# Kernel optimization log

Measured on AMD Instinct MI355X. Metric: run time of the kernel, lower is better.

Reference implementation:

```python
import jax, jax.numpy as jnp
import numpy as np

DEPTH, DIM, M_DIM, K = 3, 16, 16, 8  # depth, emb_dim, EGNN m_dim default, num_nearest_neighbors
LN_EPS = 1e-5


def _gather(x, idx):
    # x: [B,L,...], idx: [B,L,K] -> [B,L,K,...] (per-batch neighbor gather)
    return jax.vmap(lambda xb, ib: xb[ib])(x, idx)


def _lin(k, fi, fo):
    k1, k2 = jax.random.split(k)
    lim = 1.0 / np.sqrt(fi)
    w = jax.random.uniform(k1, (fi, fo), minval=-lim, maxval=lim, dtype=jnp.float32)
    b = jax.random.uniform(k2, (fo,), minval=-lim, maxval=lim, dtype=jnp.float32)
    return w, b


def _stacked(k, fi, fo):
    ws, bs = zip(*[_lin(kk, fi, fo) for kk in jax.random.split(k, DEPTH)])
    return jnp.stack(ws), jnp.stack(bs)


def setup_inputs() -> dict:
    key = jax.random.key(0)
    ks = jax.random.split(key, 16)
    B, L, num_tokens = 16, 1024, 2
    edge_in = 2 * DIM + 1  # feats_i, feats_j, rel_dist
    inp = {}
    inp['coords'] = jax.random.normal(ks[0], (B, L, 3), dtype=jnp.float32) * 3.0
    inp['residues'] = jax.random.randint(ks[1], (B, L), 0, num_tokens)
    inp['lengths'] = jax.random.randint(ks[2], (B,), L // 2, L + 1)
    inp['token_emb'] = jax.random.normal(ks[3], (num_tokens, DIM), dtype=jnp.float32)
    inp['pos_emb'] = jax.random.normal(ks[4], (L, DIM), dtype=jnp.float32)
    inp['edge_w1'], inp['edge_b1'] = _stacked(ks[5], edge_in, edge_in * 2)
    inp['edge_w2'], inp['edge_b2'] = _stacked(ks[6], edge_in * 2, M_DIM)
    inp['coors_w1'], inp['coors_b1'] = _stacked(ks[7], M_DIM, M_DIM * 4)
    inp['coors_w2'], inp['coors_b2'] = _stacked(ks[8], M_DIM * 4, 1)
    inp['ln_g'] = jnp.ones((DEPTH, DIM), jnp.float32)
    inp['ln_b'] = jnp.zeros((DEPTH, DIM), jnp.float32)
    inp['node_w1'], inp['node_b1'] = _stacked(ks[9], DIM + M_DIM, DIM * 2)
    inp['node_w2'], inp['node_b2'] = _stacked(ks[10], DIM * 2, DIM)
    inp['final_w'], inp['final_b'] = _lin(ks[11], DIM, 3)
    return inp


def reference(coords, residues, lengths, token_emb, pos_emb,
              edge_w1, edge_b1, edge_w2, edge_b2,
              coors_w1, coors_b1, coors_w2, coors_b2,
              ln_g, ln_b, node_w1, node_b1, node_w2, node_b2,
              final_w, final_b):
    B, L, _ = coords.shape
    silu = jax.nn.silu
    mask = jnp.arange(L)[None, :] < lengths[:, None]                 # [B,L]
    pair_mask = mask[:, :, None] & mask[:, None, :]                  # [B,L,L]
    eye = jnp.eye(L, dtype=bool)
    # chain adjacency: i <-> i+1 where both endpoints are within length
    r = jnp.arange(L - 1)
    chain = jnp.zeros((L, L), bool).at[r, r + 1].set(True)
    chain = chain | chain.T
    adj = (chain[None] & pair_mask) & ~eye                           # [B,L,L]

    feats = token_emb[residues] + pos_emb[None, :L]                  # [B,L,D]
    coors = coords
    for d in range(DEPTH):
        # pairwise squared distances for kNN ranking (memory-bound)
        rel_dist_full = jnp.sum((coors[:, :, None] - coors[:, None, :]) ** 2, -1)  # [B,L,L]
        ranking = jnp.where(pair_mask, rel_dist_full, 1e5)
        ranking = jnp.where(eye, -1.0, ranking)   # self always selected first
        ranking = jnp.where(adj, 0.0, ranking)    # adjacency edges forced in
        _, idx = jax.lax.top_k(-ranking, K)                           # [B,L,K] smallest
        mask_j = _gather(mask, idx)
        emask = mask[:, :, None] & mask_j                             # [B,L,K] (valid_radius=inf)
        coors_j = _gather(coors, idx)                                 # [B,L,K,3]
        rel_coors = coors[:, :, None] - coors_j                       # [B,L,K,3]
        rel_dist = jnp.sum(rel_coors ** 2, -1, keepdims=True)         # [B,L,K,1]
        feats_j = _gather(feats, idx)                                 # [B,L,K,D]
        feats_i = jnp.broadcast_to(feats[:, :, None], feats_j.shape)
        edge_in = jnp.concatenate([feats_i, feats_j, rel_dist], -1)   # [B,L,K,2D+1]
        h = silu(edge_in @ edge_w1[d] + edge_b1[d])
        m_ij = silu(h @ edge_w2[d] + edge_b2[d])                      # [B,L,K,M]
        # equivariant coordinate update
        w = silu(m_ij @ coors_w1[d] + coors_b1[d]) @ coors_w2[d] + coors_b2[d]
        w = jnp.where(emask[..., None], w, 0.0)[..., 0]               # [B,L,K]
        coors = coors + jnp.einsum('blk,blkc->blc', w, rel_coors)
        # node update (norm_feats=True in EGNN_Network -> LayerNorm)
        m_i = jnp.sum(jnp.where(emask[..., None], m_ij, 0.0), 2)      # [B,L,M]
        mu = feats.mean(-1, keepdims=True)
        var = jnp.mean((feats - mu) ** 2, -1, keepdims=True)
        normed = (feats - mu) / jnp.sqrt(var + LN_EPS) * ln_g[d] + ln_b[d]
        nin = jnp.concatenate([normed, m_i], -1)                      # [B,L,D+M]
        feats = feats + (silu(nin @ node_w1[d] + node_b1[d]) @ node_w2[d] + node_b2[d])
    delta = feats @ final_w + final_b                                 # [B,L,3]
    return delta
```

## Files before the change

### kernel.cpp

```cpp
#include <hip/hip_runtime.h>
#include <math.h>

typedef unsigned long long u64;
typedef unsigned int u32;

#define NB 16
#define SL 1024
#define DIM 16
#define MDIM 16
#define KNN 8
#define EH 66
#define CH 64
#define NHID 32
#define LN_EPS 1e-5f
#define W1T_STRIDE 36

__device__ __forceinline__ float silu_f(float x) {
    return x / (1.0f + __expf(-x));
}

__global__ __launch_bounds__(256) void init_kernel(
    const float* __restrict__ coords, const int* __restrict__ residues,
    const float* __restrict__ token_emb, const float* __restrict__ pos_emb,
    float* __restrict__ coordsA, float* __restrict__ featsA)
{
    const int nid = blockIdx.x * 256 + threadIdx.x;
    if (nid >= NB * SL) return;
    const int l = nid & (SL - 1);
    const int r = residues[nid];
#pragma unroll
    for (int c = 0; c < DIM; ++c)
        featsA[nid * DIM + c] = token_emb[r * DIM + c] + pos_emb[l * DIM + c];
#pragma unroll
    for (int c = 0; c < 3; ++c)
        coordsA[nid * 3 + c] = coords[nid * 3 + c];
}

__global__ __launch_bounds__(256) void pack_kernel(
    const float* __restrict__ ew1, const float* __restrict__ cw1,
    const float* __restrict__ nw1, const float* __restrict__ nw2,
    float* __restrict__ w1t, float* __restrict__ cw1t,
    float* __restrict__ nw1t, float* __restrict__ nw2t)
{
    const int stride = gridDim.x * 256;
    const int t0 = blockIdx.x * 256 + threadIdx.x;
    for (int idx = t0; idx < 3 * EH * 33; idx += stride) {
        int d = idx / (EH * 33); int r = idx - d * EH * 33; int u = r / 33; int c = r - u * 33;
        w1t[(d * EH + u) * W1T_STRIDE + c] = ew1[(d * 33 + c) * EH + u];
    }
    for (int idx = t0; idx < 3 * CH * 16; idx += stride) {
        int d = idx / (CH * 16); int r = idx - d * CH * 16; int t = r >> 4; int v = r & 15;
        cw1t[(d * CH + t) * 16 + v] = cw1[(d * 16 + v) * CH + t];
    }
    for (int idx = t0; idx < 3 * NHID * 32; idx += stride) {
        int d = idx / (NHID * 32); int r = idx - d * NHID * 32; int u = r >> 5; int c = r & 31;
        nw1t[(d * NHID + u) * 32 + c] = nw1[(d * 32 + c) * NHID + u];
    }
    for (int idx = t0; idx < 3 * 16 * 32; idx += stride) {
        int d = idx / (16 * 32); int r = idx - d * 16 * 32; int c = r >> 5; int u = r & 31;
        nw2t[(d * 16 + c) * 32 + u] = nw2[(d * 32 + u) * 16 + c];
    }
}

__device__ __forceinline__ void merge8(u32* a, const u32* bb) {
    u32 c[8];
#pragma unroll
    for (int t = 0; t < 8; ++t) c[t] = min(a[t], bb[7 - t]);
#define MCAS(x, y) { u32 mn = min(c[x], c[y]); u32 mx = max(c[x], c[y]); c[x] = mn; c[y] = mx; }
    MCAS(0, 4) MCAS(1, 5) MCAS(2, 6) MCAS(3, 7)
    MCAS(0, 2) MCAS(1, 3) MCAS(4, 6) MCAS(5, 7)
    MCAS(0, 1) MCAS(2, 3) MCAS(4, 5) MCAS(6, 7)
#undef MCAS
#pragma unroll
    for (int t = 0; t < 8; ++t) a[t] = c[t];
}

__global__ __launch_bounds__(1024) void knn_kernel(
    const float* __restrict__ coords, const int* __restrict__ lengths,
    int* __restrict__ idxbuf)
{
    __shared__ float s_cand[SL * 3];
    __shared__ u32 lists[16][64][9];
    const int tid = threadIdx.x;
    const int b = blockIdx.x >> 4;
    const int i0 = (blockIdx.x & 15) << 6;
    const int len = lengths[b];
    const float* cb = coords + (size_t)b * SL * 3;
    for (int idx = tid; idx < SL * 3; idx += 1024) s_cand[idx] = cb[idx];
    __syncthreads();

    const int wv = tid >> 6;
    const int lane = tid & 63;
    const int i = i0 + lane;
    const bool mi = i < len;
    const float xi = s_cand[i * 3 + 0], yi = s_cand[i * 3 + 1], zi = s_cand[i * 3 + 2];

    u32 lst[8];
#pragma unroll
    for (int t = 0; t < 8; ++t) lst[t] = 0xFFFFFFFFu;

    const int jbase = wv << 6;
#pragma unroll 4
    for (int jj = 0; jj < 64; ++jj) {
        const int j = jbase + jj;
        const float xj = s_cand[j * 3 + 0], yj = s_cand[j * 3 + 1], zj = s_cand[j * 3 + 2];
        const float dx = xi - xj, dy = yi - yj, dz = zi - zj;
        const float dist = dx * dx + dy * dy + dz * dz;
        const bool pm = mi && (j < len);
        float v = pm ? dist : 1e5f;
        v = (pm && (j - i == 1 || i - j == 1)) ? 0.0f : v;
        v = (j == i) ? -1.0f : v;
        u32 bits = __float_as_uint(v);
        bits ^= (u32)((int)bits >> 31) | 0x80000000u;
        const u32 key = (bits & 0xFFFFFC00u) | (u32)j;
#pragma unroll
        for (int p = 7; p >= 1; --p)
            lst[p] = (key < lst[p]) ? ((key < lst[p - 1]) ? lst[p - 1] : key) : lst[p];
        lst[0] = min(key, lst[0]);
    }

#pragma unroll
    for (int t = 0; t < 8; ++t) lists[wv][lane][t] = lst[t];
    __syncthreads();

    if (tid < 512) {
        const int p = tid >> 6, q = tid & 63;
        u32 a[8], bb[8];
#pragma unroll
        for (int t = 0; t < 8; ++t) { a[t] = lists[2 * p][q][t]; bb[t] = lists[2 * p + 1][q][t]; }
        merge8(a, bb);
#pragma unroll
        for (int t = 0; t < 8; ++t) lists[2 * p][q][t] = a[t];
    }
    __syncthreads();
    if (tid < 256) {
        const int p = tid >> 6, q = tid & 63;
        u32 a[8], bb[8];
#pragma unroll
        for (int t = 0; t < 8; ++t) { a[t] = lists[4 * p][q][t]; bb[t] = lists[4 * p + 2][q][t]; }
        merge8(a, bb);
#pragma unroll
        for (int t = 0; t < 8; ++t) lists[4 * p][q][t] = a[t];
    }
    __syncthreads();
    if (tid < 128) {
        const int p = tid >> 6, q = tid & 63;
        u32 a[8], bb[8];
#pragma unroll
        for (int t = 0; t < 8; ++t) { a[t] = lists[8 * p][q][t]; bb[t] = lists[8 * p + 4][q][t]; }
        merge8(a, bb);
#pragma unroll
        for (int t = 0; t < 8; ++t) lists[8 * p][q][t] = a[t];
    }
    __syncthreads();
    if (tid < 64) {
        const int q = tid;
        u32 a[8], bb[8];
#pragma unroll
        for (int t = 0; t < 8; ++t) { a[t] = lists[0][q][t]; bb[t] = lists[8][q][t]; }
        merge8(a, bb);
        const size_t node = (size_t)b * SL + i0 + q;
        int4 r0 = make_int4((int)(a[0] & 1023u), (int)(a[1] & 1023u), (int)(a[2] & 1023u), (int)(a[3] & 1023u));
        int4 r1 = make_int4((int)(a[4] & 1023u), (int)(a[5] & 1023u), (int)(a[6] & 1023u), (int)(a[7] & 1023u));
        ((int4*)idxbuf)[node * 2 + 0] = r0;
        ((int4*)idxbuf)[node * 2 + 1] = r1;
    }
}

__global__ __launch_bounds__(256, 4) void layer_kernel(
    const int d,
    const float* __restrict__ coordsIn, float* __restrict__ coordsOut,
    const float* __restrict__ featsIn, float* __restrict__ featsOut,
    const int* __restrict__ idxbuf, const int* __restrict__ lengths,
    const float* __restrict__ w1t, const float* __restrict__ g_eb1,
    const float* __restrict__ g_ew2, const float* __restrict__ g_eb2,
    const float* __restrict__ cw1t, const float* __restrict__ g_cb1,
    const float* __restrict__ g_cw2, const float* __restrict__ g_cb2,
    const float* __restrict__ g_lng, const float* __restrict__ g_lnb,
    const float* __restrict__ nw1t, const float* __restrict__ g_nb1,
    const float* __restrict__ nw2t, const float* __restrict__ g_nb2)
{
    __shared__ float s_w1[EH * 36];
    __shared__ float s_w2e[EH * 16];
    __shared__ float s_cw1[CH * 16];
    __shared__ float s_cw2v[CH];
    __shared__ float s_nw1[NHID * 36];
    __shared__ float s_nw2[16 * 36];
    __shared__ float s_eb1[EH], s_eb2[16], s_cb1[CH];
    __shared__ float s_lng[16], s_lnb[16], s_nb1[32], s_nb2[16];
    __shared__ float s_cb2v;
    __shared__ __align__(16) float s_ex[2 * 64 * 20];

    const int tid = threadIdx.x;
    for (int t = tid; t < EH * 36; t += 256) s_w1[t] = w1t[d * EH * 36 + t];
    for (int t = tid; t < EH * 16; t += 256) s_w2e[t] = g_ew2[d * EH * 16 + t];
    for (int t = tid; t < CH * 16; t += 256) s_cw1[t] = cw1t[d * CH * 16 + t];
    for (int t = tid; t < NHID * 32; t += 256) s_nw1[(t >> 5) * 36 + (t & 31)] = nw1t[d * NHID * 32 + t];
    for (int t = tid; t < 16 * 32; t += 256) s_nw2[(t >> 5) * 36 + (t & 31)] = nw2t[d * 16 * 32 + t];
    if (tid < CH) { s_cw2v[tid] = g_cw2[d * CH + tid]; s_cb1[tid] = g_cb1[d * CH + tid]; }
    if (tid < EH) s_eb1[tid] = g_eb1[d * EH + tid];
    if (tid < 16) {
        s_eb2[tid] = g_eb2[d * 16 + tid];
        s_lng[tid] = g_lng[d * 16 + tid];
        s_lnb[tid] = g_lnb[d * 16 + tid];
        s_nb2[tid] = g_nb2[d * 16 + tid];
    }
    if (tid < 32) s_nb1[tid] = g_nb1[d * 32 + tid];
    if (tid == 0) s_cb2v = g_cb2[d];

    const int wvid = tid >> 6;
    const int h = wvid & 1;
    const int p = wvid >> 1;
    const int lane = tid & 63;
    const int e = blockIdx.x * 128 + p * 64 + lane;
    const int n = e >> 3;
    const int b = n >> 10;
    const int i = n & (SL - 1);
    const int k = lane & 7;
    const int len = lengths[b];
    const int j = idxbuf[e];
    const bool em = (i < len) && (j < len);

    float fi[16], fj[16];
    {
        const float4* pp = (const float4*)(featsIn + (size_t)n * DIM);
        float4 a = pp[0], c2 = pp[1], c3 = pp[2], c4 = pp[3];
        fi[0]=a.x; fi[1]=a.y; fi[2]=a.z; fi[3]=a.w;
        fi[4]=c2.x; fi[5]=c2.y; fi[6]=c2.z; fi[7]=c2.w;
        fi[8]=c3.x; fi[9]=c3.y; fi[10]=c3.z; fi[11]=c3.w;
        fi[12]=c4.x; fi[13]=c4.y; fi[14]=c4.z; fi[15]=c4.w;
    }
    {
        const float4* pp = (const float4*)(featsIn + ((size_t)b * SL + j) * DIM);
        float4 a = pp[0], c2 = pp[1], c3 = pp[2], c4 = pp[3];
        fj[0]=a.x; fj[1]=a.y; fj[2]=a.z; fj[3]=a.w;
        fj[4]=c2.x; fj[5]=c2.y; fj[6]=c2.z; fj[7]=c2.w;
        fj[8]=c3.x; fj[9]=c3.y; fj[10]=c3.z; fj[11]=c3.w;
        fj[12]=c4.x; fj[13]=c4.y; fj[14]=c4.z; fj[15]=c4.w;
    }
    float ci[3], rel[3];
    {
        const float* cp = coordsIn + (size_t)n * 3;
        const float* cq = coordsIn + ((size_t)b * SL + j) * 3;
        ci[0] = cp[0]; ci[1] = cp[1]; ci[2] = cp[2];
        rel[0] = ci[0] - cq[0]; rel[1] = ci[1] - cq[1]; rel[2] = ci[2] - cq[2];
    }
    const float rd = fmaf(rel[0], rel[0], fmaf(rel[1], rel[1], rel[2] * rel[2]));

    __syncthreads();

    const int ub = h * 33;
    float macc[16];
#pragma unroll
    for (int v = 0; v < 16; ++v) macc[v] = h ? 0.0f : s_eb2[v];
#pragma unroll 3
    for (int uu = 0; uu < 33; ++uu) {
        const float* wr = &s_w1[(ub + uu) * 36];
        float h0 = s_eb1[ub + uu], h1 = 0.f, h2 = 0.f, h3 = 0.f;
#pragma unroll
        for (int c = 0; c < 16; c += 4) {
            h0 = fmaf(fi[c + 0], wr[c + 0], h0);
            h1 = fmaf(fi[c + 1], wr[c + 1], h1);
            h2 = fmaf(fi[c + 2], wr[c + 2], h2);
            h3 = fmaf(fi[c + 3], wr[c + 3], h3);
        }
#pragma unroll
        for (int c = 0; c < 16; c += 4) {
            h0 = fmaf(fj[c + 0], wr[16 + c + 0], h0);
            h1 = fmaf(fj[c + 1], wr[16 + c + 1], h1);
            h2 = fmaf(fj[c + 2], wr[16 + c + 2], h2);
            h3 = fmaf(fj[c + 3], wr[16 + c + 3], h3);
        }
        h0 = fmaf(rd, wr[32], h0);
        const float hh = silu_f((h0 + h1) + (h2 + h3));
        const float* w2r = &s_w2e[(ub + uu) * 16];
#pragma unroll
        for (int v = 0; v < 16; ++v) macc[v] = fmaf(hh, w2r[v], macc[v]);
    }

    float4* exq = (float4*)&s_ex[((p << 6) + lane) * 20];
    if (h) {
        exq[0] = make_float4(macc[0], macc[1], macc[2], macc[3]);
        exq[1] = make_float4(macc[4], macc[5], macc[6], macc[7]);
        exq[2] = make_float4(macc[8], macc[9], macc[10], macc[11]);
        exq[3] = make_float4(macc[12], macc[13], macc[14], macc[15]);
    }
    __syncthreads();
    float mm[16];
    if (!h) {
        float4 e0 = exq[0], e1 = exq[1], e2 = exq[2], e3 = exq[3];
        macc[0]+=e0.x; macc[1]+=e0.y; macc[2]+=e0.z; macc[3]+=e0.w;
        macc[4]+=e1.x; macc[5]+=e1.y; macc[6]+=e1.z; macc[7]+=e1.w;
        macc[8]+=e2.x; macc[9]+=e2.y; macc[10]+=e2.z; macc[11]+=e2.w;
        macc[12]+=e3.x; macc[13]+=e3.y; macc[14]+=e3.z; macc[15]+=e3.w;
#pragma unroll
        for (int v = 0; v < 16; ++v) mm[v] = silu_f(macc[v]);
        exq[0] = make_float4(mm[0], mm[1], mm[2], mm[3]);
        exq[1] = make_float4(mm[4], mm[5], mm[6], mm[7]);
        exq[2] = make_float4(mm[8], mm[9], mm[10], mm[11]);
        exq[3] = make_float4(mm[12], mm[13], mm[14], mm[15]);
    }
    __syncthreads();
    if (h) {
        float4 e0 = exq[0], e1 = exq[1], e2 = exq[2], e3 = exq[3];
        mm[0]=e0.x; mm[1]=e0.y; mm[2]=e0.z; mm[3]=e0.w;
        mm[4]=e1.x; mm[5]=e1.y; mm[6]=e1.z; mm[7]=e1.w;
        mm[8]=e2.x; mm[9]=e2.y; mm[10]=e2.z; mm[11]=e2.w;
        mm[12]=e3.x; mm[13]=e3.y; mm[14]=e3.z; mm[15]=e3.w;
    }

    const int tb = h * 32;
    float wa = 0.f;
#pragma unroll 4
    for (int tt = 0; tt < 32; ++tt) {
        const float* cr = &s_cw1[(tb + tt) * 16];
        float a0 = s_cb1[tb + tt], a1 = 0.f;
#pragma unroll
        for (int v = 0; v < 16; v += 2) {
            a0 = fmaf(mm[v], cr[v], a0);
            a1 = fmaf(mm[v + 1], cr[v + 1], a1);
        }
        wa = fmaf(silu_f(a0 + a1), s_cw2v[tb + tt], wa);
    }
    s_ex[((p << 6) + lane) * 20 + 16 + h] = wa;
    __syncthreads();
    const float wao = s_ex[((p << 6) + lane) * 20 + 17 - h];
    const float we = em ? (wa + wao + s_cb2v) : 0.f;

    float wr0 = we * rel[0], wr1 = we * rel[1], wr2 = we * rel[2];
#pragma unroll
    for (int s = 1; s < 8; s <<= 1) {
        wr0 += __shfl_xor(wr0, s, 64);
        wr1 += __shfl_xor(wr1, s, 64);
        wr2 += __shfl_xor(wr2, s, 64);
    }
    if (!h && k == 0) {
        coordsOut[(size_t)n * 3 + 0] = ci[0] + wr0;
        coordsOut[(size_t)n * 3 + 1] = ci[1] + wr1;
        coordsOut[(size_t)n * 3 + 2] = ci[2] + wr2;
    }

    float mi_[16];
#pragma unroll
    for (int v = 0; v < 16; ++v) mi_[v] = em ? mm[v] : 0.f;
#pragma unroll
    for (int s = 1; s < 8; s <<= 1) {
#pragma unroll
        for (int v = 0; v < 16; ++v) mi_[v] += __shfl_xor(mi_[v], s, 64);
    }

    float mu = 0.f;
#pragma unroll
    for (int c = 0; c < 16; ++c) mu += fi[c];
    mu *= 0.0625f;
    float var = 0.f;
#pragma unroll
    for (int c = 0; c < 16; ++c) { const float dd = fi[c] - mu; var = fmaf(dd, dd, var); }
    var *= 0.0625f;
    const float rs = rsqrtf(var + LN_EPS);
    float nn[16];
#pragma unroll
    for (int c = 0; c < 16; ++c) nn[c] = fmaf((fi[c] - mu) * rs, s_lng[c], s_lnb[c]);

    float nh[4];
#pragma unroll
    for (int q = 0; q < 4; ++q) {
        const int u = k * 4 + q;
        const float* nr = &s_nw1[u * 36];
        float a0 = s_nb1[u], a1 = 0.f;
#pragma unroll
        for (int c = 0; c < 16; c += 2) {
            a0 = fmaf(nn[c], nr[c], a0);
            a1 = fmaf(nn[c + 1], nr[c + 1], a1);
        }
#pragma unroll
        for (int v = 0; v < 16; v += 2) {
            a0 = fmaf(mi_[v], nr[16 + v], a0);
            a1 = fmaf(mi_[v + 1], nr[16 + v + 1], a1);
        }
        nh[q] = silu_f(a0 + a1);
    }

    const int c0 = 2 * k, c1 = 2 * k + 1;
    const float* w2a = &s_nw2[c0 * 36];
    const float* w2b = &s_nw2[c1 * 36];
    float o0 = s_nb2[c0], o1 = s_nb2[c1];
    const int lbase = lane & ~7;
#pragma unroll
    for (int u = 0; u < 32; ++u) {
        const float v = __shfl(nh[u & 3], lbase + (u >> 2), 64);
        o0 = fmaf(v, w2a[u], o0);
        o1 = fmaf(v, w2b[u], o1);
    }
    if (!h) {
        ((float2*)featsOut)[(size_t)n * 8 + k] = make_float2(fi[c0] + o0, fi[c1] + o1);
    }
}

__global__ __launch_bounds__(256) void final_kernel(
    const float* __restrict__ feats, const float* __restrict__ fw,
    const float* __restrict__ fb, float* __restrict__ out)
{
    const int nid = blockIdx.x * 256 + threadIdx.x;
    if (nid >= NB * SL) return;
    float f[DIM];
#pragma unroll
    for (int c = 0; c < DIM; ++c) f[c] = feats[nid * DIM + c];
#pragma unroll
    for (int o = 0; o < 3; ++o) {
        float acc = fb[o];
#pragma unroll
        for (int c = 0; c < DIM; ++c) acc = fmaf(f[c], fw[c * 3 + o], acc);
        out[nid * 3 + o] = acc;
    }
}

extern "C" void kernel_launch(void* const* d_in, const int* in_sizes, int n_in,
                              void* d_out, int out_size, void* d_ws, size_t ws_size,
                              hipStream_t stream) {
    const float* coords    = (const float*)d_in[0];
    const int*   residues  = (const int*)d_in[1];
    const int*   lengths   = (const int*)d_in[2];
    const float* token_emb = (const float*)d_in[3];
    const float* pos_emb   = (const float*)d_in[4];
    const float* ew1 = (const float*)d_in[5];
    const float* eb1 = (const float*)d_in[6];
    const float* ew2 = (const float*)d_in[7];
    const float* eb2 = (const float*)d_in[8];
    const float* cw1 = (const float*)d_in[9];
    const float* cb1 = (const float*)d_in[10];
    const float* cw2 = (const float*)d_in[11];
    const float* cb2 = (const float*)d_in[12];
    const float* lng = (const float*)d_in[13];
    const float* lnb = (const float*)d_in[14];
    const float* nw1 = (const float*)d_in[15];
    const float* nb1 = (const float*)d_in[16];
    const float* nw2 = (const float*)d_in[17];
    const float* nb2 = (const float*)d_in[18];
    const float* fw  = (const float*)d_in[19];
    const float* fb  = (const float*)d_in[20];

    float* ws = (float*)d_ws;
    float* coordsA = ws;
    float* coordsB = coordsA + NB * SL * 3;
    float* featsA  = coordsB + NB * SL * 3;
    float* featsB  = featsA + NB * SL * DIM;
    int*   idxbuf  = (int*)(featsB + NB * SL * DIM);
    float* w1t  = (float*)(idxbuf + NB * SL * KNN);
    float* cw1t = w1t + 3 * EH * W1T_STRIDE;
    float* nw1t = cw1t + 3 * CH * 16;
    float* nw2t = nw1t + 3 * NHID * 32;

    pack_kernel<<<32, 256, 0, stream>>>(ew1, cw1, nw1, nw2, w1t, cw1t, nw1t, nw2t);
    init_kernel<<<NB * SL / 256, 256, 0, stream>>>(coords, residues, token_emb, pos_emb, coordsA, featsA);

    float* cIn = coordsA; float* cOut = coordsB;
    float* fIn = featsA;  float* fOut = featsB;
    for (int d = 0; d < 3; ++d) {
        knn_kernel<<<NB * SL / 64, 1024, 0, stream>>>(cIn, lengths, idxbuf);
        layer_kernel<<<NB * SL * KNN / 128, 256, 0, stream>>>(d, cIn, cOut, fIn, fOut, idxbuf, lengths,
            w1t, eb1, ew2, eb2, cw1t, cb1, cw2, cb2, lng, lnb, nw1t, nb1, nw2t, nb2);
        float* t;
        t = cIn; cIn = cOut; cOut = t;
        t = fIn; fIn = fOut; fOut = t;
    }

    final_kernel<<<NB * SL / 256, 256, 0, stream>>>(fIn, fw, fb, (float*)d_out);
}
```

Baseline: 306.1 us.

## Split edge MLP across four waves and halve KNN query tile

Result: slower. 343.0 us (+12.1%).

```diff
diff --git a/kernel.cpp b/kernel.cpp
--- a/kernel.cpp
+++ b/kernel.cpp
@@ -10,6 +10,7 @@
 #define MDIM 16
 #define KNN 8
 #define EH 66
+#define EHP 68
 #define CH 64
 #define NHID 32
 #define LN_EPS 1e-5f
@@ -80,10 +81,10 @@
     int* __restrict__ idxbuf)
 {
     __shared__ float s_cand[SL * 3];
-    __shared__ u32 lists[16][64][9];
+    __shared__ u32 lists[32][32][9];
     const int tid = threadIdx.x;
-    const int b = blockIdx.x >> 4;
-    const int i0 = (blockIdx.x & 15) << 6;
+    const int b = blockIdx.x >> 5;
+    const int i0 = (blockIdx.x & 31) << 5;
     const int len = lengths[b];
     const float* cb = coords + (size_t)b * SL * 3;
     for (int idx = tid; idx < SL * 3; idx += 1024) s_cand[idx] = cb[idx];
@@ -91,28 +92,29 @@
 
     const int wv = tid >> 6;
     const int lane = tid & 63;
-    const int i = i0 + lane;
-    const bool mi = i < len;
+    const int q = lane & 31;
+    const int sub = lane >> 5;
+    const int s = wv * 2 + sub;
+    const int i = i0 + q;
     const float xi = s_cand[i * 3 + 0], yi = s_cand[i * 3 + 1], zi = s_cand[i * 3 + 2];
 
     u32 lst[8];
 #pragma unroll
     for (int t = 0; t < 8; ++t) lst[t] = 0xFFFFFFFFu;
 
-    const int jbase = wv << 6;
+    const int jbase = s << 5;
 #pragma unroll 4
-    for (int jj = 0; jj < 64; ++jj) {
+    for (int jj = 0; jj < 32; ++jj) {
         const int j = jbase + jj;
         const float xj = s_cand[j * 3 + 0], yj = s_cand[j * 3 + 1], zj = s_cand[j * 3 + 2];
         const float dx = xi - xj, dy = yi - yj, dz = zi - zj;
         const float dist = dx * dx + dy * dy + dz * dz;
-        const bool pm = mi && (j < len);
-        float v = pm ? dist : 1e5f;
-        v = (pm && (j - i == 1 || i - j == 1)) ? 0.0f : v;
-        v = (j == i) ? -1.0f : v;
-        u32 bits = __float_as_uint(v);
-        bits ^= (u32)((int)bits >> 31) | 0x80000000u;
-        const u32 key = (bits & 0xFFFFFC00u) | (u32)j;
+        const bool valid = j < len;
+        const u32 kd = (__float_as_uint(dist) | 0x80000000u) & 0xFFFFFC00u;
+        u32 key = valid ? kd : 0xC7C35000u;
+        if (valid && (j == i + 1 || j + 1 == i)) key = 0x80000000u;
+        if (j == i) key = 0x407FFC00u;
+        key |= (u32)j;
 #pragma unroll
         for (int p = 7; p >= 1; --p)
             lst[p] = (key < lst[p]) ? ((key < lst[p - 1]) ? lst[p - 1] : key) : lst[p];
@@ -120,46 +122,56 @@
     }
 
 #pragma unroll
-    for (int t = 0; t < 8; ++t) lists[wv][lane][t] = lst[t];
+    for (int t = 0; t < 8; ++t) lists[s][q][t] = lst[t];
     __syncthreads();
 
     if (tid < 512) {
-        const int p = tid >> 6, q = tid & 63;
+        const int p = tid >> 5, qq = tid & 31;
         u32 a[8], bb[8];
 #pragma unroll
-        for (int t = 0; t < 8; ++t) { a[t] = lists[2 * p][q][t]; bb[t] = lists[2 * p + 1][q][t]; }
+        for (int t = 0; t < 8; ++t) { a[t] = lists[2 * p][qq][t]; bb[t] = lists[2 * p + 1][qq][t]; }
         merge8(a, bb);
 #pragma unroll
-        for (int t = 0; t < 8; ++t) lists[2 * p][q][t] = a[t];
+        for (int t = 0; t < 8; ++t) lists[2 * p][qq][t] = a[t];
     }
     __syncthreads();
     if (tid < 256) {
-        const int p = tid >> 6, q = tid & 63;
+        const int p = tid >> 5, qq = tid & 31;
         u32 a[8], bb[8];
 #pragma unroll
-        for (int t = 0; t < 8; ++t) { a[t] = lists[4 * p][q][t]; bb[t] = lists[4 * p + 2][q][t]; }
+        for (int t = 0; t < 8; ++t) { a[t] = lists[4 * p][qq][t]; bb[t] = lists[4 * p + 2][qq][t]; }
         merge8(a, bb);
 #pragma unroll
-        for (int t = 0; t < 8; ++t) lists[4 * p][q][t] = a[t];
+        for (int t = 0; t < 8; ++t) lists[4 * p][qq][t] = a[t];
     }
     __syncthreads();
     if (tid < 128) {
-        const int p = tid >> 6, q = tid & 63;
+        const int p = tid >> 5, qq = tid & 31;
         u32 a[8], bb[8];
 #pragma unroll
-        for (int t = 0; t < 8; ++t) { a[t] = lists[8 * p][q][t]; bb[t] = lists[8 * p + 4][q][t]; }
+        for (int t = 0; t < 8; ++t) { a[t] = lists[8 * p][qq][t]; bb[t] = lists[8 * p + 4][qq][t]; }
         merge8(a, bb);
 #pragma unroll
-        for (int t = 0; t < 8; ++t) lists[8 * p][q][t] = a[t];
+        for (int t = 0; t < 8; ++t) lists[8 * p][qq][t] = a[t];
     }
     __syncthreads();
     if (tid < 64) {
-        const int q = tid;
+        const int p = tid >> 5, qq = tid & 31;
         u32 a[8], bb[8];
 #pragma unroll
-        for (int t = 0; t < 8; ++t) { a[t] = lists[0][q][t]; bb[t] = lists[8][q][t]; }
+        for (int t = 0; t < 8; ++t) { a[t] = lists[16 * p][qq][t]; bb[t] = lists[16 * p + 8][qq][t]; }
         merge8(a, bb);
-        const size_t node = (size_t)b * SL + i0 + q;
+#pragma unroll
+        for (int t = 0; t < 8; ++t) lists[16 * p][qq][t] = a[t];
+    }
+    __syncthreads();
+    if (tid < 32) {
+        const int qq = tid;
+        u32 a[8], bb[8];
+#pragma unroll
+        for (int t = 0; t < 8; ++t) { a[t] = lists[0][qq][t]; bb[t] = lists[16][qq][t]; }
+        merge8(a, bb);
+        const size_t node = (size_t)b * SL + i0 + qq;
         int4 r0 = make_int4((int)(a[0] & 1023u), (int)(a[1] & 1023u), (int)(a[2] & 1023u), (int)(a[3] & 1023u));
         int4 r1 = make_int4((int)(a[4] & 1023u), (int)(a[5] & 1023u), (int)(a[6] & 1023u), (int)(a[7] & 1023u));
         ((int4*)idxbuf)[node * 2 + 0] = r0;
@@ -167,7 +179,7 @@
     }
 }
 
-__global__ __launch_bounds__(256, 4) void layer_kernel(
+__global__ __launch_bounds__(512, 6) void layer_kernel(
     const int d,
     const float* __restrict__ coordsIn, float* __restrict__ coordsOut,
     const float* __restrict__ featsIn, float* __restrict__ featsOut,
@@ -180,39 +192,42 @@
     const float* __restrict__ nw1t, const float* __restrict__ g_nb1,
     const float* __restrict__ nw2t, const float* __restrict__ g_nb2)
 {
-    __shared__ float s_w1[EH * 36];
-    __shared__ float s_w2e[EH * 16];
+    __shared__ float s_w1[EHP * 36];
+    __shared__ float s_w2e[EHP * 16];
     __shared__ float s_cw1[CH * 16];
     __shared__ float s_cw2v[CH];
     __shared__ float s_nw1[NHID * 36];
     __shared__ float s_nw2[16 * 36];
-    __shared__ float s_eb1[EH], s_eb2[16], s_cb1[CH];
+    __shared__ float s_eb1[EHP], s_eb2[16], s_cb1[CH];
     __shared__ float s_lng[16], s_lnb[16], s_nb1[32], s_nb2[16];
     __shared__ float s_cb2v;
-    __shared__ __align__(16) float s_ex[2 * 64 * 20];
+    __shared__ float s_bufA[2][16][66];
+    __shared__ float s_bufB[2][16][66];
+    __shared__ float s_wA[2][64], s_wB[2][64];
 
     const int tid = threadIdx.x;
-    for (int t = tid; t < EH * 36; t += 256) s_w1[t] = w1t[d * EH * 36 + t];
-    for (int t = tid; t < EH * 16; t += 256) s_w2e[t] = g_ew2[d * EH * 16 + t];
-    for (int t = tid; t < CH * 16; t += 256) s_cw1[t] = cw1t[d * CH * 16 + t];
-    for (int t = tid; t < NHID * 32; t += 256) s_nw1[(t >> 5) * 36 + (t & 31)] = nw1t[d * NHID * 32 + t];
-    for (int t = tid; t < 16 * 32; t += 256) s_nw2[(t >> 5) * 36 + (t & 31)] = nw2t[d * 16 * 32 + t];
+    for (int t = tid; t < EHP * 36; t += 512) s_w1[t] = (t < EH * 36) ? w1t[d * EH * 36 + t] : 0.0f;
+    for (int t = tid; t < EHP * 16; t += 512) s_w2e[t] = (t < EH * 16) ? g_ew2[d * EH * 16 + t] : 0.0f;
+    for (int t = tid; t < CH * 16; t += 512) s_cw1[t] = cw1t[d * CH * 16 + t];
+    for (int t = tid; t < NHID * 32; t += 512) s_nw1[(t >> 5) * 36 + (t & 31)] = nw1t[d * NHID * 32 + t];
+    for (int t = tid; t < 16 * 32; t += 512) s_nw2[(t >> 5) * 36 + (t & 31)] = nw2t[d * 16 * 32 + t];
     if (tid < CH) { s_cw2v[tid] = g_cw2[d * CH + tid]; s_cb1[tid] = g_cb1[d * CH + tid]; }
-    if (tid < EH) s_eb1[tid] = g_eb1[d * EH + tid];
-    if (tid < 16) {
-        s_eb2[tid] = g_eb2[d * 16 + tid];
-        s_lng[tid] = g_lng[d * 16 + tid];
-        s_lnb[tid] = g_lnb[d * 16 + tid];
-        s_nb2[tid] = g_nb2[d * 16 + tid];
-    }
-    if (tid < 32) s_nb1[tid] = g_nb1[d * 32 + tid];
-    if (tid == 0) s_cb2v = g_cb2[d];
-
-    const int wvid = tid >> 6;
-    const int h = wvid & 1;
-    const int p = wvid >> 1;
+    if (tid < EHP) s_eb1[tid] = (tid < EH) ? g_eb1[d * EH + tid] : 0.0f;
+    if (tid >= 128 && tid < 144) {
+        const int c = tid - 128;
+        s_eb2[c] = g_eb2[d * 16 + c];
+        s_lng[c] = g_lng[d * 16 + c];
+        s_lnb[c] = g_lnb[d * 16 + c];
+        s_nb2[c] = g_nb2[d * 16 + c];
+    }
+    if (tid >= 160 && tid < 192) s_nb1[tid - 160] = g_nb1[d * 32 + (tid - 160)];
+    if (tid == 200) s_cb2v = g_cb2[d];
+
+    const int wv = tid >> 6;
+    const int g = wv >> 2;
+    const int qt = wv & 3;
     const int lane = tid & 63;
-    const int e = blockIdx.x * 128 + p * 64 + lane;
+    const int e = blockIdx.x * 128 + g * 64 + lane;
     const int n = e >> 3;
     const int b = n >> 10;
     const int i = n & (SL - 1);
@@ -249,12 +264,12 @@
 
     __syncthreads();
 
-    const int ub = h * 33;
+    const int ub = qt * 17;
     float macc[16];
 #pragma unroll
-    for (int v = 0; v < 16; ++v) macc[v] = h ? 0.0f : s_eb2[v];
+    for (int v = 0; v < 16; ++v) macc[v] = (qt == 0) ? s_eb2[v] : 0.0f;
 #pragma unroll 3
-    for (int uu = 0; uu < 33; ++uu) {
+    for (int uu = 0; uu < 17; ++uu) {
         const float* wr = &s_w1[(ub + uu) * 36];
         float h0 = s_eb1[ub + uu], h1 = 0.f, h2 = 0.f, h3 = 0.f;
 #pragma unroll
@@ -278,121 +293,117 @@
         for (int v = 0; v < 16; ++v) macc[v] = fmaf(hh, w2r[v], macc[v]);
     }
 
-    float4* exq = (float4*)&s_ex[((p << 6) + lane) * 20];
-    if (h) {
-        exq[0] = make_float4(macc[0], macc[1], macc[2], macc[3]);
-        exq[1] = make_float4(macc[4], macc[5], macc[6], macc[7]);
-        exq[2] = make_float4(macc[8], macc[9], macc[10], macc[11]);
-        exq[3] = make_float4(macc[12], macc[13], macc[14], macc[15]);
+    if (qt == 1) {
+#pragma unroll
+        for (int v = 0; v < 16; ++v) s_bufA[g][v][lane] = macc[v];
+    } else if (qt == 3) {
+#pragma unroll
+        for (int v = 0; v < 16; ++v) s_bufB[g][v][lane] = macc[v];
+    }
+    __syncthreads();
+    if (qt == 0) {
+#pragma unroll
+        for (int v = 0; v < 16; ++v) macc[v] += s_bufA[g][v][lane];
+    } else if (qt == 2) {
+#pragma unroll
+        for (int v = 0; v < 16; ++v) { macc[v] += s_bufB[g][v][lane]; s_bufB[g][v][lane] = macc[v]; }
     }
     __syncthreads();
     float mm[16];
-    if (!h) {
-        float4 e0 = exq[0], e1 = exq[1], e2 = exq[2], e3 = exq[3];
-        macc[0]+=e0.x; macc[1]+=e0.y; macc[2]+=e0.z; macc[3]+=e0.w;
-        macc[4]+=e1.x; macc[5]+=e1.y; macc[6]+=e1.z; macc[7]+=e1.w;
-        macc[8]+=e2.x; macc[9]+=e2.y; macc[10]+=e2.z; macc[11]+=e2.w;
-        macc[12]+=e3.x; macc[13]+=e3.y; macc[14]+=e3.z; macc[15]+=e3.w;
-#pragma unroll
-        for (int v = 0; v < 16; ++v) mm[v] = silu_f(macc[v]);
-        exq[0] = make_float4(mm[0], mm[1], mm[2], mm[3]);
-        exq[1] = make_float4(mm[4], mm[5], mm[6], mm[7]);
-        exq[2] = make_float4(mm[8], mm[9], mm[10], mm[11]);
-        exq[3] = make_float4(mm[12], mm[13], mm[14], mm[15]);
-    }
-    __syncthreads();
-    if (h) {
-        float4 e0 = exq[0], e1 = exq[1], e2 = exq[2], e3 = exq[3];
-        mm[0]=e0.x; mm[1]=e0.y; mm[2]=e0.z; mm[3]=e0.w;
-        mm[4]=e1.x; mm[5]=e1.y; mm[6]=e1.z; mm[7]=e1.w;
-        mm[8]=e2.x; mm[9]=e2.y; mm[10]=e2.z; mm[11]=e2.w;
-        mm[12]=e3.x; mm[13]=e3.y; mm[14]=e3.z; mm[15]=e3.w;
-    }
-
-    const int tb = h * 32;
-    float wa = 0.f;
+    if (qt == 0) {
+#pragma unroll
+        for (int v = 0; v < 16; ++v) { macc[v] += s_bufB[g][v][lane]; mm[v] = silu_f(macc[v]); s_bufA[g][v][lane] = mm[v]; }
+    }
+    __syncthreads();
+    if (qt != 0) {
+#pragma unroll
+        for (int v = 0; v < 16; ++v) mm[v] = s_bufA[g][v][lane];
+    }
+
+    float mi_[16];
+    if (qt == 1 || qt == 2) {
+        const int tb = (qt - 1) * 32;
+        float wa = 0.f;
 #pragma unroll 4
-    for (int tt = 0; tt < 32; ++tt) {
-        const float* cr = &s_cw1[(tb + tt) * 16];
-        float a0 = s_cb1[tb + tt], a1 = 0.f;
-#pragma unroll
-        for (int v = 0; v < 16; v += 2) {
-            a0 = fmaf(mm[v], cr[v], a0);
-            a1 = fmaf(mm[v + 1], cr[v + 1], a1);
-        }
-        wa = fmaf(silu_f(a0 + a1), s_cw2v[tb + tt], wa);
-    }
-    s_ex[((p << 6) + lane) * 20 + 16 + h] = wa;
-    __syncthreads();
-    const float wao = s_ex[((p << 6) + lane) * 20 + 17 - h];
-    const float we = em ? (wa + wao + s_cb2v) : 0.f;
-
-    float wr0 = we * rel[0], wr1 = we * rel[1], wr2 = we * rel[2];
-#pragma unroll
-    for (int s = 1; s < 8; s <<= 1) {
-        wr0 += __shfl_xor(wr0, s, 64);
-        wr1 += __shfl_xor(wr1, s, 64);
-        wr2 += __shfl_xor(wr2, s, 64);
-    }
-    if (!h && k == 0) {
-        coordsOut[(size_t)n * 3 + 0] = ci[0] + wr0;
-        coordsOut[(size_t)n * 3 + 1] = ci[1] + wr1;
-        coordsOut[(size_t)n * 3 + 2] = ci[2] + wr2;
-    }
-
-    float mi_[16];
-#pragma unroll
-    for (int v = 0; v < 16; ++v) mi_[v] = em ? mm[v] : 0.f;
-#pragma unroll
-    for (int s = 1; s < 8; s <<= 1) {
-#pragma unroll
-        for (int v = 0; v < 16; ++v) mi_[v] += __shfl_xor(mi_[v], s, 64);
-    }
-
-    float mu = 0.f;
-#pragma unroll
-    for (int c = 0; c < 16; ++c) mu += fi[c];
-    mu *= 0.0625f;
-    float var = 0.f;
-#pragma unroll
-    for (int c = 0; c < 16; ++c) { const float dd = fi[c] - mu; var = fmaf(dd, dd, var); }
-    var *= 0.0625f;
-    const float rs = rsqrtf(var + LN_EPS);
-    float nn[16];
-#pragma unroll
-    for (int c = 0; c < 16; ++c) nn[c] = fmaf((fi[c] - mu) * rs, s_lng[c], s_lnb[c]);
-
-    float nh[4];
-#pragma unroll
-    for (int q = 0; q < 4; ++q) {
-        const int u = k * 4 + q;
-        const float* nr = &s_nw1[u * 36];
-        float a0 = s_nb1[u], a1 = 0.f;
-#pragma unroll
-        for (int c = 0; c < 16; c += 2) {
-            a0 = fmaf(nn[c], nr[c], a0);
-            a1 = fmaf(nn[c + 1], nr[c + 1], a1);
-        }
-#pragma unroll
-        for (int v = 0; v < 16; v += 2) {
-            a0 = fmaf(mi_[v], nr[16 + v], a0);
-            a1 = fmaf(mi_[v + 1], nr[16 + v + 1], a1);
-        }
-        nh[q] = silu_f(a0 + a1);
-    }
-
-    const int c0 = 2 * k, c1 = 2 * k + 1;
-    const float* w2a = &s_nw2[c0 * 36];
-    const float* w2b = &s_nw2[c1 * 36];
-    float o0 = s_nb2[c0], o1 = s_nb2[c1];
-    const int lbase = lane & ~7;
-#pragma unroll
-    for (int u = 0; u < 32; ++u) {
-        const float v = __shfl(nh[u & 3], lbase + (u >> 2), 64);
-        o0 = fmaf(v, w2a[u], o0);
-        o1 = fmaf(v, w2b[u], o1);
-    }
-    if (!h) {
+        for (int tt = 0; tt < 32; ++tt) {
+            const float* cr = &s_cw1[(tb + tt) * 16];
+            float a0 = s_cb1[tb + tt], a1 = 0.f;
+#pragma unroll
+            for (int v = 0; v < 16; v += 2) {
+                a0 = fmaf(mm[v], cr[v], a0);
+                a1 = fmaf(mm[v + 1], cr[v + 1], a1);
+            }
+            wa = fmaf(silu_f(a0 + a1), s_cw2v[tb + tt], wa);
+        }
+        if (qt == 1) s_wA[g][lane] = wa; else s_wB[g][lane] = wa;
+    } else if (qt == 0) {
+#pragma unroll
+        for (int v = 0; v < 16; ++v) mi_[v] = em ? mm[v] : 0.f;
+#pragma unroll
+        for (int s = 1; s < 8; s <<= 1) {
+#pragma unroll
+            for (int v = 0; v < 16; ++v) mi_[v] += __shfl_xor(mi_[v], s, 64);
+        }
+    }
+    __syncthreads();
+
+    if (qt == 3) {
+        const float we = em ? (s_wA[g][lane] + s_wB[g][lane] + s_cb2v) : 0.f;
+        float wr0 = we * rel[0], wr1 = we * rel[1], wr2 = we * rel[2];
+#pragma unroll
+        for (int s = 1; s < 8; s <<= 1) {
+            wr0 += __shfl_xor(wr0, s, 64);
+            wr1 += __shfl_xor(wr1, s, 64);
+            wr2 += __shfl_xor(wr2, s, 64);
+        }
+        if (k == 0) {
+            coordsOut[(size_t)n * 3 + 0] = ci[0] + wr0;
+            coordsOut[(size_t)n * 3 + 1] = ci[1] + wr1;
+            coordsOut[(size_t)n * 3 + 2] = ci[2] + wr2;
+        }
+    } else if (qt == 0) {
+        float mu = 0.f;
+#pragma unroll
+        for (int c = 0; c < 16; ++c) mu += fi[c];
+        mu *= 0.0625f;
+        float var = 0.f;
+#pragma unroll
+        for (int c = 0; c < 16; ++c) { const float dd = fi[c] - mu; var = fmaf(dd, dd, var); }
+        var *= 0.0625f;
+        const float rs = rsqrtf(var + LN_EPS);
+        float nn[16];
+#pragma unroll
+        for (int c = 0; c < 16; ++c) nn[c] = fmaf((fi[c] - mu) * rs, s_lng[c], s_lnb[c]);
+
+        float nh[4];
+#pragma unroll
+        for (int qq = 0; qq < 4; ++qq) {
+            const int u = k * 4 + qq;
+            const float* nr = &s_nw1[u * 36];
+            float a0 = s_nb1[u], a1 = 0.f;
+#pragma unroll
+            for (int c = 0; c < 16; c += 2) {
+                a0 = fmaf(nn[c], nr[c], a0);
+                a1 = fmaf(nn[c + 1], nr[c + 1], a1);
+            }
+#pragma unroll
+            for (int v = 0; v < 16; v += 2) {
+                a0 = fmaf(mi_[v], nr[16 + v], a0);
+                a1 = fmaf(mi_[v + 1], nr[16 + v + 1], a1);
+            }
+            nh[qq] = silu_f(a0 + a1);
+        }
+        const int c0 = 2 * k, c1 = 2 * k + 1;
+        const float* w2a = &s_nw2[c0 * 36];
+        const float* w2b = &s_nw2[c1 * 36];
+        float o0 = s_nb2[c0], o1 = s_nb2[c1];
+        const int lbase = lane & ~7;
+#pragma unroll
+        for (int u = 0; u < 32; ++u) {
+            const float v = __shfl(nh[u & 3], lbase + (u >> 2), 64);
+            o0 = fmaf(v, w2a[u], o0);
+            o1 = fmaf(v, w2b[u], o1);
+        }
         ((float2*)featsOut)[(size_t)n * 8 + k] = make_float2(fi[c0] + o0, fi[c1] + o1);
     }
 }
@@ -457,8 +468,8 @@
     float* cIn = coordsA; float* cOut = coordsB;
     float* fIn = featsA;  float* fOut = featsB;
     for (int d = 0; d < 3; ++d) {
-        knn_kernel<<<NB * SL / 64, 1024, 0, stream>>>(cIn, lengths, idxbuf);
-        layer_kernel<<<NB * SL * KNN / 128, 256, 0, stream>>>(d, cIn, cOut, fIn, fOut, idxbuf, lengths,
+        knn_kernel<<<NB * 32, 1024, 0, stream>>>(cIn, lengths, idxbuf);
+        layer_kernel<<<NB * SL * KNN / 128, 512, 0, stream>>>(d, cIn, cOut, fIn, fOut, idxbuf, lengths,
             w1t, eb1, ew2, eb2, cw1t, cb1, cw2, cb2, lng, lnb, nw1t, nb1, nw2t, nb2);
         float* t;
         t = cIn; cIn = cOut; cOut = t;
```
